# Kernel tuning notes

Hardware: AMD Instinct MI355X
Metric: run time of the kernel (lower is better)

Reference implementation:

```python
import jax, jax.numpy as jnp
import numpy as np

WS = (8, 8)            # window_size
NUM_HEADS = 8


def _rel_pos_index():
    # Faithful to the torch buffer construction (meshgrid indexing='ij').
    ch, cw = np.arange(WS[0]), np.arange(WS[1])
    coords = np.stack(np.meshgrid(ch, cw, indexing='ij')).reshape(2, -1)  # (2, N)
    rel = coords[:, :, None] - coords[:, None, :]                          # (2, N, N)
    rel = rel.transpose(1, 2, 0).copy()                                    # (N, N, 2)
    rel[..., 0] += WS[0] - 1
    rel[..., 1] += WS[1] - 1
    rel[..., 0] *= 2 * WS[1] - 1
    return jnp.asarray(rel.sum(-1))                                        # (N, N) int


def setup_inputs() -> dict:
    key = jax.random.key(0)
    ks = jax.random.split(key, 7)
    B_, C, N, nW = 4096, 256, 64, 4096  # B_ = batch(1) * num_windows(4096)
    return {
        "x": jax.random.normal(ks[0], (B_, C, N), jnp.float32),
        "mask": jax.random.normal(ks[1], (nW, N, N), jnp.float32),
        "qkv_w": jax.random.normal(ks[2], (3 * C, C), jnp.float32) * 0.05,
        "qkv_b": jax.random.normal(ks[3], (3 * C,), jnp.float32) * 0.02,
        "proj_w": jax.random.normal(ks[4], (C, C), jnp.float32) * 0.05,
        "proj_b": jax.random.normal(ks[5], (C,), jnp.float32) * 0.02,
        "bias_table": jax.random.normal(ks[6], ((2 * WS[0] - 1) * (2 * WS[1] - 1), NUM_HEADS), jnp.float32) * 0.02,
    }


def reference(x, mask, qkv_w, qkv_b, proj_w, proj_b, bias_table):
    B_, C, N = x.shape
    H = NUM_HEADS
    hd = C // H
    scale = hd ** -0.5

    # Conv1d kernel_size=1 == linear over the channel dim.
    qkv = jnp.einsum('bcn,dc->bdn', x, qkv_w) + qkv_b[None, :, None]   # (B_, 3C, N)
    qkv = qkv.reshape(B_, 3, H, hd, N)
    q, k, v = qkv[:, 0], qkv[:, 1], qkv[:, 2]                          # (B_, H, hd, N)

    attn = jnp.einsum('bhdn,bhdm->bhnm', q * scale, k)                 # (B_, H, N, N)

    rpi = _rel_pos_index()                                              # (N, N)
    bias = bias_table[rpi]                                              # (N, N, H) gather
    attn = attn + jnp.transpose(bias, (2, 0, 1))[None]                  # (B_, H, N, N)

    nW = mask.shape[0]
    attn = (attn.reshape(B_ // nW, nW, H, N, N) + mask[None, :, None]).reshape(B_, H, N, N)
    attn = jax.nn.softmax(attn, axis=-1)

    out = jnp.einsum('bhnm,bhdm->bnhd', attn, v).reshape(B_, N, C)      # (B_, N, C)
    return jnp.einsum('bnc,dc->bnd', out, proj_w) + proj_b              # (B_, N, C)
```

## Files before the change

### kernel.cpp

```cpp
#include <hip/hip_runtime.h>

typedef __bf16 bf16_t;
typedef bf16_t bf16x8 __attribute__((ext_vector_type(8)));
typedef bf16_t bf16x4 __attribute__((ext_vector_type(4)));
typedef float  f32x4  __attribute__((ext_vector_type(4)));

#define NWIN 4096
#define CDIM 256
#define NTOK 64
#define NH   8
#define HDIM 32

#define OFF_Q 0
#define OFF_K 40960
#define OFF_V 81920
#define OFF_X 118784
#define LDS_BYTES 152576

__device__ __forceinline__ f32x4 mfma16(bf16x8 a, bf16x8 b, f32x4 c) {
    return __builtin_amdgcn_mfma_f32_16x16x32_bf16(a, b, c, 0, 0, 0);
}

template<bool USE_WS>
__launch_bounds__(512, 2)
__global__ void win_attn_kernel(const float* __restrict__ x,
                                const float* __restrict__ mask,
                                const float* __restrict__ qkv_w,
                                const float* __restrict__ qkv_b,
                                const float* __restrict__ proj_w,
                                const float* __restrict__ proj_b,
                                const float* __restrict__ bias_table,
                                const bf16_t* __restrict__ qkv_wb,
                                const bf16_t* __restrict__ proj_wb,
                                float* __restrict__ out)
{
    __shared__ __attribute__((aligned(16))) unsigned char smem[LDS_BYTES];
    bf16_t* q_lds    = (bf16_t*)(smem + OFF_Q);
    bf16_t* k_lds    = (bf16_t*)(smem + OFF_K);
    bf16_t* v_lds    = (bf16_t*)(smem + OFF_V);
    bf16_t* xs       = (bf16_t*)(smem + OFF_X);
    float*  mask_lds = (float*) (smem + OFF_X);
    bf16_t* o_lds    = (bf16_t*)(smem + OFF_K);

    const int b    = blockIdx.x;
    const int tid  = threadIdx.x;
    const int w    = tid >> 6;
    const int lane = tid & 63;
    const int quad = lane >> 4;
    const int l15  = lane & 15;

    {
        const float* xb = x + (size_t)b * (CDIM * NTOK);
        #pragma unroll
        for (int it = 0; it < 8; ++it) {
            int i  = (tid + it * 512) * 4;
            int c  = i >> 6;
            int n0 = i & 63;
            f32x4 v4 = *(const f32x4*)(xb + i);
            #pragma unroll
            for (int j = 0; j < 4; ++j)
                xs[(n0 + j) * 264 + c] = (bf16_t)v4[j];
        }
    }
    __syncthreads();

    {
        f32x4 acc[6][4];
        #pragma unroll
        for (int rt = 0; rt < 6; ++rt)
            #pragma unroll
            for (int ct = 0; ct < 4; ++ct)
                acc[rt][ct] = (f32x4){0.f, 0.f, 0.f, 0.f};

        const int row_base = w * 96;
        for (int kk = 0; kk < 8; ++kk) {
            const int c0 = kk * 32;
            bf16x8 afr[6];
            #pragma unroll
            for (int rt = 0; rt < 6; ++rt) {
                int row = row_base + rt * 16 + l15;
                if constexpr (USE_WS) {
                    afr[rt] = *(const bf16x8*)(qkv_wb + row * CDIM + c0 + quad * 8);
                } else {
                    const float* ap = qkv_w + row * CDIM + c0 + quad * 8;
                    f32x4 a0 = *(const f32x4*)ap;
                    f32x4 a1 = *(const f32x4*)(ap + 4);
                    bf16x8 t;
                    #pragma unroll
                    for (int j = 0; j < 4; ++j) { t[j] = (bf16_t)a0[j]; t[j + 4] = (bf16_t)a1[j]; }
                    afr[rt] = t;
                }
            }
            bf16x8 bfr[4];
            #pragma unroll
            for (int ct = 0; ct < 4; ++ct)
                bfr[ct] = *(const bf16x8*)(xs + (ct * 16 + l15) * 264 + c0 + quad * 8);
            #pragma unroll
            for (int rt = 0; rt < 6; ++rt)
                #pragma unroll
                for (int ct = 0; ct < 4; ++ct)
                    acc[rt][ct] = mfma16(afr[rt], bfr[ct], acc[rt][ct]);
        }
        #pragma unroll
        for (int rt = 0; rt < 6; ++rt) {
            int r0  = row_base + rt * 16;
            int rq  = r0 + quad * 4;
            f32x4 b4 = *(const f32x4*)(qkv_b + rq);
            int sec = r0 >> 8;
            int h   = (r0 & 255) >> 5;
            int dd0 = rq & 31;
            #pragma unroll
            for (int ct = 0; ct < 4; ++ct) {
                int n = ct * 16 + l15;
                if (sec == 2) {
                    bf16_t* dst = v_lds + h * (32 * 72) + n;
                    #pragma unroll
                    for (int r = 0; r < 4; ++r)
                        dst[(dd0 + r) * 72] = (bf16_t)(acc[rt][ct][r] + b4[r]);
                } else {
                    bf16_t* dst = (sec == 0 ? q_lds : k_lds) + h * (64 * 40) + n * 40 + dd0;
                    bf16x4 pk;
                    #pragma unroll
                    for (int r = 0; r < 4; ++r) pk[r] = (bf16_t)(acc[rt][ct][r] + b4[r]);
                    *(bf16x4*)dst = pk;
                }
            }
        }
    }
    __syncthreads();

    {
        const float* mb = mask + (size_t)b * (NTOK * NTOK);
        #pragma unroll
        for (int it = 0; it < 2; ++it) {
            int i = (tid + it * 512) * 4;
            *(f32x4*)(mask_lds + i) = *(const f32x4*)(mb + i);
        }
    }

    const int h = w;
    f32x4 sacc[4][4];
    #pragma unroll
    for (int rt = 0; rt < 4; ++rt)
        #pragma unroll
        for (int ct = 0; ct < 4; ++ct)
            sacc[rt][ct] = (f32x4){0.f, 0.f, 0.f, 0.f};
    {
        bf16x8 qa[4], kb[4];
        #pragma unroll
        for (int rt = 0; rt < 4; ++rt)
            qa[rt] = *(const bf16x8*)(q_lds + h * 2560 + (rt * 16 + l15) * 40 + quad * 8);
        #pragma unroll
        for (int ct = 0; ct < 4; ++ct)
            kb[ct] = *(const bf16x8*)(k_lds + h * 2560 + (ct * 16 + l15) * 40 + quad * 8);
        #pragma unroll
        for (int rt = 0; rt < 4; ++rt)
            #pragma unroll
            for (int ct = 0; ct < 4; ++ct)
                sacc[rt][ct] = mfma16(qa[rt], kb[ct], sacc[rt][ct]);
    }
    __syncthreads();

    {
        const float scale = 0.17677669529663687f;
        int mh[4], mw[4], mcol[4];
        #pragma unroll
        for (int ct = 0; ct < 4; ++ct) {
            int m = ct * 16 + l15;
            mcol[ct] = m; mh[ct] = m >> 3; mw[ct] = m & 7;
        }
        #pragma unroll
        for (int rt = 0; rt < 4; ++rt) {
            #pragma unroll
            for (int reg = 0; reg < 4; ++reg) {
                int n  = rt * 16 + quad * 4 + reg;
                int nh = n >> 3, nw = n & 7;
                float l[4];
                #pragma unroll
                for (int ct = 0; ct < 4; ++ct) {
                    int idx = (nh - mh[ct] + 7) * 15 + (nw - mw[ct] + 7);
                    float bias = bias_table[idx * NH + h];
                    l[ct] = sacc[rt][ct][reg] * scale + bias + mask_lds[n * 64 + mcol[ct]];
                }
                float mx = fmaxf(fmaxf(l[0], l[1]), fmaxf(l[2], l[3]));
                #pragma unroll
                for (int d = 1; d < 16; d <<= 1) mx = fmaxf(mx, __shfl_xor(mx, d, 64));
                float s = 0.f;
                #pragma unroll
                for (int ct = 0; ct < 4; ++ct) { l[ct] = __expf(l[ct] - mx); s += l[ct]; }
                #pragma unroll
                for (int d = 1; d < 16; d <<= 1) s += __shfl_xor(s, d, 64);
                float inv = 1.0f / s;
                #pragma unroll
                for (int ct = 0; ct < 4; ++ct) sacc[rt][ct][reg] = l[ct] * inv;
            }
        }
    }

    f32x4 oacc[4][2];
    #pragma unroll
    for (int rt = 0; rt < 4; ++rt)
        #pragma unroll
        for (int cd = 0; cd < 2; ++cd)
            oacc[rt][cd] = (f32x4){0.f, 0.f, 0.f, 0.f};
    {
        bf16_t* p_lds = q_lds + h * 2560;
        #pragma unroll
        for (int ch = 0; ch < 2; ++ch) {
            #pragma unroll
            for (int rt = 0; rt < 4; ++rt)
                #pragma unroll
                for (int reg = 0; reg < 4; ++reg) {
                    int n = rt * 16 + quad * 4 + reg;
                    p_lds[n * 40 + l15]      = (bf16_t)sacc[rt][2 * ch][reg];
                    p_lds[n * 40 + 16 + l15] = (bf16_t)sacc[rt][2 * ch + 1][reg];
                }
            #pragma unroll
            for (int rt = 0; rt < 4; ++rt) {
                bf16x8 pa = *(const bf16x8*)(p_lds + (rt * 16 + l15) * 40 + quad * 8);
                #pragma unroll
                for (int cd = 0; cd < 2; ++cd) {
                    bf16x8 vb = *(const bf16x8*)(v_lds + h * 2304 + (cd * 16 + l15) * 72 + ch * 32 + quad * 8);
                    oacc[rt][cd] = mfma16(pa, vb, oacc[rt][cd]);
                }
            }
        }
    }
    __syncthreads();

    #pragma unroll
    for (int rt = 0; rt < 4; ++rt)
        #pragma unroll
        for (int cd = 0; cd < 2; ++cd) {
            int c = h * 32 + cd * 16 + l15;
            #pragma unroll
            for (int reg = 0; reg < 4; ++reg) {
                int n = rt * 16 + quad * 4 + reg;
                o_lds[n * 264 + c] = (bf16_t)oacc[rt][cd][reg];
            }
        }
    __syncthreads();

    {
        f32x4 yacc[2][4];
        #pragma unroll
        for (int rt = 0; rt < 2; ++rt)
            #pragma unroll
            for (int ct = 0; ct < 4; ++ct)
                yacc[rt][ct] = (f32x4){0.f, 0.f, 0.f, 0.f};

        for (int kk = 0; kk < 8; ++kk) {
            const int c0 = kk * 32;
            bf16x8 afr[2];
            #pragma unroll
            for (int rt = 0; rt < 2; ++rt) {
                int e = w * 32 + rt * 16 + l15;
                if constexpr (USE_WS) {
                    afr[rt] = *(const bf16x8*)(proj_wb + e * CDIM + c0 + quad * 8);
                } else {
                    const float* ap = proj_w + e * CDIM + c0 + quad * 8;
                    f32x4 a0 = *(const f32x4*)ap;
                    f32x4 a1 = *(const f32x4*)(ap + 4);
                    bf16x8 t;
                    #pragma unroll
                    for (int j = 0; j < 4; ++j) { t[j] = (bf16_t)a0[j]; t[j + 4] = (bf16_t)a1[j]; }
                    afr[rt] = t;
                }
            }
            bf16x8 bfr[4];
            #pragma unroll
            for (int ct = 0; ct < 4; ++ct)
                bfr[ct] = *(const bf16x8*)(o_lds + (ct * 16 + l15) * 264 + c0 + quad * 8);
            #pragma unroll
            for (int rt = 0; rt < 2; ++rt)
                #pragma unroll
                for (int ct = 0; ct < 4; ++ct)
                    yacc[rt][ct] = mfma16(afr[rt], bfr[ct], yacc[rt][ct]);
        }
        float* ob = out + (size_t)b * (NTOK * CDIM);
        #pragma unroll
        for (int rt = 0; rt < 2; ++rt) {
            int e0 = w * 32 + rt * 16 + quad * 4;
            f32x4 pb4 = *(const f32x4*)(proj_b + e0);
            #pragma unroll
            for (int ct = 0; ct < 4; ++ct) {
                int n = ct * 16 + l15;
                f32x4 r = yacc[rt][ct] + pb4;
                *(f32x4*)(ob + n * 256 + e0) = r;
            }
        }
    }
}

__global__ void cvt_weights(const float* __restrict__ qkv_w,
                            const float* __restrict__ proj_w,
                            bf16_t* __restrict__ qkv_wb,
                            bf16_t* __restrict__ proj_wb)
{
    int i = blockIdx.x * 256 + threadIdx.x;
    int base = i * 4;
    const float* src; bf16_t* dst;
    if (base < 196608) { src = qkv_w + base; dst = qkv_wb + base; }
    else { base -= 196608; src = proj_w + base; dst = proj_wb + base; }
    f32x4 v = *(const f32x4*)src;
    bf16x4 o;
    #pragma unroll
    for (int j = 0; j < 4; ++j) o[j] = (bf16_t)v[j];
    *(bf16x4*)dst = o;
}

extern "C" void kernel_launch(void* const* d_in, const int* in_sizes, int n_in,
                              void* d_out, int out_size, void* d_ws, size_t ws_size,
                              hipStream_t stream) {
    const float* x          = (const float*)d_in[0];
    const float* mask       = (const float*)d_in[1];
    const float* qkv_w      = (const float*)d_in[2];
    const float* qkv_b      = (const float*)d_in[3];
    const float* proj_w     = (const float*)d_in[4];
    const float* proj_b     = (const float*)d_in[5];
    const float* bias_table = (const float*)d_in[6];
    float* out = (float*)d_out;

    const size_t ws_needed = (size_t)(196608 + 65536) * sizeof(bf16_t);
    if (ws_size >= ws_needed) {
        bf16_t* qkv_wb  = (bf16_t*)d_ws;
        bf16_t* proj_wb = qkv_wb + 196608;
        cvt_weights<<<256, 256, 0, stream>>>(qkv_w, proj_w, qkv_wb, proj_wb);
        win_attn_kernel<true><<<NWIN, 512, 0, stream>>>(
            x, mask, qkv_w, qkv_b, proj_w, proj_b, bias_table, qkv_wb, proj_wb, out);
    } else {
        win_attn_kernel<false><<<NWIN, 512, 0, stream>>>(
            x, mask, qkv_w, qkv_b, proj_w, proj_b, bias_table, nullptr, nullptr, out);
    }
}
```

Baseline: 886.2 us.

## Assign each wave one head's QKV rows and keep Q/K/V in registers

Each wave now computes the Q, K and V projection rows for its own head, so the shared Q/K/V LDS buffers go away and each wave transposes through a small private scratch area without block barriers. LDS usage drops to about 58 KB, which allows the launch bound to request four blocks per CU instead of two. The change also folds the scale into Q, computes S transposed so the softmax reduction needs only two shuffles, defers normalisation to the output, and changes the x load pattern. The costs are higher register pressure from holding all per-head accumulators and possible spilling at the higher occupancy target.

Result: slower. 1.418 ms (+60.0%).

```diff
diff --git a/kernel.cpp b/kernel.cpp
--- a/kernel.cpp
+++ b/kernel.cpp
@@ -9,20 +9,16 @@
 #define CDIM 256
 #define NTOK 64
 #define NH   8
-#define HDIM 32
-
-#define OFF_Q 0
-#define OFF_K 40960
-#define OFF_V 81920
-#define OFF_X 118784
-#define LDS_BYTES 152576
+
+#define OFF_MASK  40960
+#define LDS_BYTES 58368
 
 __device__ __forceinline__ f32x4 mfma16(bf16x8 a, bf16x8 b, f32x4 c) {
     return __builtin_amdgcn_mfma_f32_16x16x32_bf16(a, b, c, 0, 0, 0);
 }
 
 template<bool USE_WS>
-__launch_bounds__(512, 2)
+__launch_bounds__(512, 4)
 __global__ void win_attn_kernel(const float* __restrict__ x,
                                 const float* __restrict__ mask,
                                 const float* __restrict__ qkv_w,
@@ -35,12 +31,9 @@
                                 float* __restrict__ out)
 {
     __shared__ __attribute__((aligned(16))) unsigned char smem[LDS_BYTES];
-    bf16_t* q_lds    = (bf16_t*)(smem + OFF_Q);
-    bf16_t* k_lds    = (bf16_t*)(smem + OFF_K);
-    bf16_t* v_lds    = (bf16_t*)(smem + OFF_V);
-    bf16_t* xs       = (bf16_t*)(smem + OFF_X);
-    float*  mask_lds = (float*) (smem + OFF_X);
-    bf16_t* o_lds    = (bf16_t*)(smem + OFF_K);
+    bf16_t* xs       = (bf16_t*)smem;
+    bf16_t* o_lds    = (bf16_t*)smem;
+    float*  mask_lds = (float*)(smem + OFF_MASK);
 
     const int b    = blockIdx.x;
     const int tid  = threadIdx.x;
@@ -48,196 +41,213 @@
     const int lane = tid & 63;
     const int quad = lane >> 4;
     const int l15  = lane & 15;
+    bf16_t* buf0 = (bf16_t*)(smem + w * 5120);
 
     {
         const float* xb = x + (size_t)b * (CDIM * NTOK);
         #pragma unroll
-        for (int it = 0; it < 8; ++it) {
-            int i  = (tid + it * 512) * 4;
-            int c  = i >> 6;
-            int n0 = i & 63;
-            f32x4 v4 = *(const f32x4*)(xb + i);
-            #pragma unroll
-            for (int j = 0; j < 4; ++j)
-                xs[(n0 + j) * 264 + c] = (bf16_t)v4[j];
+        for (int cb = 0; cb < 4; ++cb) {
+            const int c0 = cb * 64 + w * 8;
+            float v[8];
+            #pragma unroll
+            for (int j = 0; j < 8; ++j) v[j] = xb[(c0 + j) * 64 + lane];
+            bf16x8 t;
+            #pragma unroll
+            for (int j = 0; j < 8; ++j) t[j] = (bf16_t)v[j];
+            *(bf16x8*)(xs + lane * 264 + c0) = t;
+        }
+        const float* mb = mask + (size_t)b * (NTOK * NTOK);
+        #pragma unroll
+        for (int it = 0; it < 2; ++it) {
+            int e = (it * 512 + tid) * 4;
+            int n = e >> 6, m = e & 63;
+            f32x4 mv = *(const f32x4*)(mb + e);
+            *(f32x4*)(mask_lds + n * 68 + m) = mv;
         }
     }
     __syncthreads();
 
+    const int h = w;
+    f32x4 aqk[4][4];
+    f32x4 av[4][2];
+    #pragma unroll
+    for (int rt = 0; rt < 4; ++rt)
+        #pragma unroll
+        for (int ct = 0; ct < 4; ++ct) aqk[rt][ct] = (f32x4){0.f,0.f,0.f,0.f};
+    #pragma unroll
+    for (int ct = 0; ct < 4; ++ct)
+        #pragma unroll
+        for (int rtl = 0; rtl < 2; ++rtl) av[ct][rtl] = (f32x4){0.f,0.f,0.f,0.f};
+
+    for (int kk = 0; kk < 8; ++kk) {
+        const int c0 = kk * 32;
+        bf16x8 afr[6];
+        #pragma unroll
+        for (int rt = 0; rt < 6; ++rt) {
+            int row = ((rt >> 1) << 8) + h * 32 + ((rt & 1) << 4) + l15;
+            if constexpr (USE_WS) {
+                afr[rt] = *(const bf16x8*)(qkv_wb + row * CDIM + c0 + quad * 8);
+            } else {
+                const float* ap = qkv_w + row * CDIM + c0 + quad * 8;
+                f32x4 a0 = *(const f32x4*)ap;
+                f32x4 a1 = *(const f32x4*)(ap + 4);
+                bf16x8 t;
+                #pragma unroll
+                for (int j = 0; j < 4; ++j) { t[j] = (bf16_t)a0[j]; t[j+4] = (bf16_t)a1[j]; }
+                afr[rt] = t;
+            }
+        }
+        bf16x8 bfr[4];
+        #pragma unroll
+        for (int ct = 0; ct < 4; ++ct)
+            bfr[ct] = *(const bf16x8*)(xs + (ct * 16 + l15) * 264 + c0 + quad * 8);
+        #pragma unroll
+        for (int rt = 0; rt < 4; ++rt)
+            #pragma unroll
+            for (int ct = 0; ct < 4; ++ct)
+                aqk[rt][ct] = mfma16(afr[rt], bfr[ct], aqk[rt][ct]);
+        #pragma unroll
+        for (int ct = 0; ct < 4; ++ct)
+            #pragma unroll
+            for (int rtl = 0; rtl < 2; ++rtl)
+                av[ct][rtl] = mfma16(bfr[ct], afr[4 + rtl], av[ct][rtl]);
+    }
+    __syncthreads();
+
+    const float scale = 0.17677669529663687f;
+
+    #pragma unroll
+    for (int rtl = 0; rtl < 2; ++rtl) {
+        f32x4 b4 = *(const f32x4*)(qkv_b + h * 32 + rtl * 16 + quad * 4);
+        #pragma unroll
+        for (int ct = 0; ct < 4; ++ct) {
+            bf16x4 pk;
+            #pragma unroll
+            for (int r = 0; r < 4; ++r) pk[r] = (bf16_t)((aqk[rtl][ct][r] + b4[r]) * scale);
+            *(bf16x4*)(buf0 + (ct * 16 + l15) * 40 + rtl * 16 + quad * 4) = pk;
+        }
+    }
+    bf16x8 qa[4];
+    #pragma unroll
+    for (int nt = 0; nt < 4; ++nt)
+        qa[nt] = *(const bf16x8*)(buf0 + (nt * 16 + l15) * 40 + quad * 8);
+
+    #pragma unroll
+    for (int rtl = 0; rtl < 2; ++rtl) {
+        f32x4 b4 = *(const f32x4*)(qkv_b + 256 + h * 32 + rtl * 16 + quad * 4);
+        #pragma unroll
+        for (int ct = 0; ct < 4; ++ct) {
+            bf16x4 pk;
+            #pragma unroll
+            for (int r = 0; r < 4; ++r) pk[r] = (bf16_t)(aqk[2 + rtl][ct][r] + b4[r]);
+            *(bf16x4*)(buf0 + (ct * 16 + l15) * 40 + rtl * 16 + quad * 4) = pk;
+        }
+    }
+    bf16x8 kb[4];
+    #pragma unroll
+    for (int mt = 0; mt < 4; ++mt)
+        kb[mt] = *(const bf16x8*)(buf0 + (mt * 16 + l15) * 40 + quad * 8);
+
+    #pragma unroll
+    for (int rtl = 0; rtl < 2; ++rtl) {
+        float bv = qkv_b[512 + h * 32 + rtl * 16 + l15];
+        #pragma unroll
+        for (int ct = 0; ct < 4; ++ct) {
+            bf16x4 pk;
+            #pragma unroll
+            for (int r = 0; r < 4; ++r) pk[r] = (bf16_t)(av[ct][rtl][r] + bv);
+            *(bf16x4*)(buf0 + (rtl * 16 + l15) * 72 + ct * 16 + quad * 4) = pk;
+        }
+    }
+
+    f32x4 sacc[4][4];
+    #pragma unroll
+    for (int mt = 0; mt < 4; ++mt)
+        #pragma unroll
+        for (int nt = 0; nt < 4; ++nt)
+            sacc[mt][nt] = mfma16(kb[mt], qa[nt], (f32x4){0.f,0.f,0.f,0.f});
+
+    float inv[4];
     {
-        f32x4 acc[6][4];
-        #pragma unroll
-        for (int rt = 0; rt < 6; ++rt)
-            #pragma unroll
-            for (int ct = 0; ct < 4; ++ct)
-                acc[rt][ct] = (f32x4){0.f, 0.f, 0.f, 0.f};
-
-        const int row_base = w * 96;
-        for (int kk = 0; kk < 8; ++kk) {
-            const int c0 = kk * 32;
-            bf16x8 afr[6];
-            #pragma unroll
-            for (int rt = 0; rt < 6; ++rt) {
-                int row = row_base + rt * 16 + l15;
-                if constexpr (USE_WS) {
-                    afr[rt] = *(const bf16x8*)(qkv_wb + row * CDIM + c0 + quad * 8);
-                } else {
-                    const float* ap = qkv_w + row * CDIM + c0 + quad * 8;
-                    f32x4 a0 = *(const f32x4*)ap;
-                    f32x4 a1 = *(const f32x4*)(ap + 4);
-                    bf16x8 t;
-                    #pragma unroll
-                    for (int j = 0; j < 4; ++j) { t[j] = (bf16_t)a0[j]; t[j + 4] = (bf16_t)a1[j]; }
-                    afr[rt] = t;
+        const int qhi = quad >> 1, qlo = quad & 1;
+        const int nwv = (l15 & 7) + 7 - 4 * qlo;
+        const int nh_ = l15 >> 3;
+        #pragma unroll
+        for (int nt = 0; nt < 4; ++nt) {
+            const int n = nt * 16 + l15;
+            #pragma unroll
+            for (int mt = 0; mt < 4; ++mt) {
+                f32x4 mv = *(const f32x4*)(mask_lds + n * 68 + mt * 16 + quad * 4);
+                int base = (nt * 2 + nh_ - 2 * mt - qhi + 7) * 15 + nwv;
+                #pragma unroll
+                for (int r = 0; r < 4; ++r)
+                    sacc[mt][nt][r] += bias_table[(base - r) * NH + h] + mv[r];
+            }
+            float mx = sacc[0][nt][0];
+            #pragma unroll
+            for (int mt = 0; mt < 4; ++mt)
+                #pragma unroll
+                for (int r = 0; r < 4; ++r) mx = fmaxf(mx, sacc[mt][nt][r]);
+            mx = fmaxf(mx, __shfl_xor(mx, 16, 64));
+            mx = fmaxf(mx, __shfl_xor(mx, 32, 64));
+            float s = 0.f;
+            #pragma unroll
+            for (int mt = 0; mt < 4; ++mt)
+                #pragma unroll
+                for (int r = 0; r < 4; ++r) {
+                    float e = __expf(sacc[mt][nt][r] - mx);
+                    sacc[mt][nt][r] = e;
+                    s += e;
                 }
-            }
-            bf16x8 bfr[4];
-            #pragma unroll
-            for (int ct = 0; ct < 4; ++ct)
-                bfr[ct] = *(const bf16x8*)(xs + (ct * 16 + l15) * 264 + c0 + quad * 8);
-            #pragma unroll
-            for (int rt = 0; rt < 6; ++rt)
-                #pragma unroll
-                for (int ct = 0; ct < 4; ++ct)
-                    acc[rt][ct] = mfma16(afr[rt], bfr[ct], acc[rt][ct]);
-        }
-        #pragma unroll
-        for (int rt = 0; rt < 6; ++rt) {
-            int r0  = row_base + rt * 16;
-            int rq  = r0 + quad * 4;
-            f32x4 b4 = *(const f32x4*)(qkv_b + rq);
-            int sec = r0 >> 8;
-            int h   = (r0 & 255) >> 5;
-            int dd0 = rq & 31;
-            #pragma unroll
-            for (int ct = 0; ct < 4; ++ct) {
-                int n = ct * 16 + l15;
-                if (sec == 2) {
-                    bf16_t* dst = v_lds + h * (32 * 72) + n;
-                    #pragma unroll
-                    for (int r = 0; r < 4; ++r)
-                        dst[(dd0 + r) * 72] = (bf16_t)(acc[rt][ct][r] + b4[r]);
-                } else {
-                    bf16_t* dst = (sec == 0 ? q_lds : k_lds) + h * (64 * 40) + n * 40 + dd0;
-                    bf16x4 pk;
-                    #pragma unroll
-                    for (int r = 0; r < 4; ++r) pk[r] = (bf16_t)(acc[rt][ct][r] + b4[r]);
-                    *(bf16x4*)dst = pk;
-                }
-            }
+            s += __shfl_xor(s, 16, 64);
+            s += __shfl_xor(s, 32, 64);
+            inv[nt] = __builtin_amdgcn_rcpf(s);
+        }
+    }
+
+    bf16x8 vb[2][2];
+    #pragma unroll
+    for (int dt = 0; dt < 2; ++dt)
+        #pragma unroll
+        for (int ch = 0; ch < 2; ++ch)
+            vb[dt][ch] = *(const bf16x8*)(buf0 + (dt * 16 + l15) * 72 + ch * 32 + quad * 8);
+
+    f32x4 oaccT[2][4];
+    #pragma unroll
+    for (int dt = 0; dt < 2; ++dt)
+        #pragma unroll
+        for (int nt = 0; nt < 4; ++nt) oaccT[dt][nt] = (f32x4){0.f,0.f,0.f,0.f};
+
+    #pragma unroll
+    for (int ch = 0; ch < 2; ++ch) {
+        #pragma unroll
+        for (int mt2 = 0; mt2 < 2; ++mt2) {
+            #pragma unroll
+            for (int nt = 0; nt < 4; ++nt) {
+                bf16x4 pk;
+                #pragma unroll
+                for (int r = 0; r < 4; ++r) pk[r] = (bf16_t)sacc[2 * ch + mt2][nt][r];
+                *(bf16x4*)(buf0 + (nt * 16 + l15) * 40 + mt2 * 16 + quad * 4) = pk;
+            }
+        }
+        #pragma unroll
+        for (int nt = 0; nt < 4; ++nt) {
+            bf16x8 pb = *(const bf16x8*)(buf0 + (nt * 16 + l15) * 40 + quad * 8);
+            #pragma unroll
+            for (int dt = 0; dt < 2; ++dt)
+                oaccT[dt][nt] = mfma16(vb[dt][ch], pb, oaccT[dt][nt]);
         }
     }
     __syncthreads();
 
-    {
-        const float* mb = mask + (size_t)b * (NTOK * NTOK);
-        #pragma unroll
-        for (int it = 0; it < 2; ++it) {
-            int i = (tid + it * 512) * 4;
-            *(f32x4*)(mask_lds + i) = *(const f32x4*)(mb + i);
-        }
-    }
-
-    const int h = w;
-    f32x4 sacc[4][4];
-    #pragma unroll
-    for (int rt = 0; rt < 4; ++rt)
-        #pragma unroll
-        for (int ct = 0; ct < 4; ++ct)
-            sacc[rt][ct] = (f32x4){0.f, 0.f, 0.f, 0.f};
-    {
-        bf16x8 qa[4], kb[4];
-        #pragma unroll
-        for (int rt = 0; rt < 4; ++rt)
-            qa[rt] = *(const bf16x8*)(q_lds + h * 2560 + (rt * 16 + l15) * 40 + quad * 8);
-        #pragma unroll
-        for (int ct = 0; ct < 4; ++ct)
-            kb[ct] = *(const bf16x8*)(k_lds + h * 2560 + (ct * 16 + l15) * 40 + quad * 8);
-        #pragma unroll
-        for (int rt = 0; rt < 4; ++rt)
-            #pragma unroll
-            for (int ct = 0; ct < 4; ++ct)
-                sacc[rt][ct] = mfma16(qa[rt], kb[ct], sacc[rt][ct]);
-    }
-    __syncthreads();
-
-    {
-        const float scale = 0.17677669529663687f;
-        int mh[4], mw[4], mcol[4];
-        #pragma unroll
-        for (int ct = 0; ct < 4; ++ct) {
-            int m = ct * 16 + l15;
-            mcol[ct] = m; mh[ct] = m >> 3; mw[ct] = m & 7;
-        }
-        #pragma unroll
-        for (int rt = 0; rt < 4; ++rt) {
-            #pragma unroll
-            for (int reg = 0; reg < 4; ++reg) {
-                int n  = rt * 16 + quad * 4 + reg;
-                int nh = n >> 3, nw = n & 7;
-                float l[4];
-                #pragma unroll
-                for (int ct = 0; ct < 4; ++ct) {
-                    int idx = (nh - mh[ct] + 7) * 15 + (nw - mw[ct] + 7);
-                    float bias = bias_table[idx * NH + h];
-                    l[ct] = sacc[rt][ct][reg] * scale + bias + mask_lds[n * 64 + mcol[ct]];
-                }
-                float mx = fmaxf(fmaxf(l[0], l[1]), fmaxf(l[2], l[3]));
-                #pragma unroll
-                for (int d = 1; d < 16; d <<= 1) mx = fmaxf(mx, __shfl_xor(mx, d, 64));
-                float s = 0.f;
-                #pragma unroll
-                for (int ct = 0; ct < 4; ++ct) { l[ct] = __expf(l[ct] - mx); s += l[ct]; }
-                #pragma unroll
-                for (int d = 1; d < 16; d <<= 1) s += __shfl_xor(s, d, 64);
-                float inv = 1.0f / s;
-                #pragma unroll
-                for (int ct = 0; ct < 4; ++ct) sacc[rt][ct][reg] = l[ct] * inv;
-            }
-        }
-    }
-
-    f32x4 oacc[4][2];
-    #pragma unroll
-    for (int rt = 0; rt < 4; ++rt)
-        #pragma unroll
-        for (int cd = 0; cd < 2; ++cd)
-            oacc[rt][cd] = (f32x4){0.f, 0.f, 0.f, 0.f};
-    {
-        bf16_t* p_lds = q_lds + h * 2560;
-        #pragma unroll
-        for (int ch = 0; ch < 2; ++ch) {
-            #pragma unroll
-            for (int rt = 0; rt < 4; ++rt)
-                #pragma unroll
-                for (int reg = 0; reg < 4; ++reg) {
-                    int n = rt * 16 + quad * 4 + reg;
-                    p_lds[n * 40 + l15]      = (bf16_t)sacc[rt][2 * ch][reg];
-                    p_lds[n * 40 + 16 + l15] = (bf16_t)sacc[rt][2 * ch + 1][reg];
-                }
-            #pragma unroll
-            for (int rt = 0; rt < 4; ++rt) {
-                bf16x8 pa = *(const bf16x8*)(p_lds + (rt * 16 + l15) * 40 + quad * 8);
-                #pragma unroll
-                for (int cd = 0; cd < 2; ++cd) {
-                    bf16x8 vb = *(const bf16x8*)(v_lds + h * 2304 + (cd * 16 + l15) * 72 + ch * 32 + quad * 8);
-                    oacc[rt][cd] = mfma16(pa, vb, oacc[rt][cd]);
-                }
-            }
-        }
-    }
-    __syncthreads();
-
-    #pragma unroll
-    for (int rt = 0; rt < 4; ++rt)
-        #pragma unroll
-        for (int cd = 0; cd < 2; ++cd) {
-            int c = h * 32 + cd * 16 + l15;
-            #pragma unroll
-            for (int reg = 0; reg < 4; ++reg) {
-                int n = rt * 16 + quad * 4 + reg;
-                o_lds[n * 264 + c] = (bf16_t)oacc[rt][cd][reg];
-            }
+    #pragma unroll
+    for (int dt = 0; dt < 2; ++dt)
+        #pragma unroll
+        for (int nt = 0; nt < 4; ++nt) {
+            bf16x4 pk;
+            #pragma unroll
+            for (int r = 0; r < 4; ++r) pk[r] = (bf16_t)(oaccT[dt][nt][r] * inv[nt]);
+            *(bf16x4*)(o_lds + (nt * 16 + l15) * 264 + h * 32 + dt * 16 + quad * 4) = pk;
         }
     __syncthreads();
 
@@ -246,8 +256,7 @@
         #pragma unroll
         for (int rt = 0; rt < 2; ++rt)
             #pragma unroll
-            for (int ct = 0; ct < 4; ++ct)
-                yacc[rt][ct] = (f32x4){0.f, 0.f, 0.f, 0.f};
+            for (int ct = 0; ct < 4; ++ct) yacc[rt][ct] = (f32x4){0.f,0.f,0.f,0.f};
 
         for (int kk = 0; kk < 8; ++kk) {
             const int c0 = kk * 32;
@@ -263,7 +272,7 @@
                     f32x4 a1 = *(const f32x4*)(ap + 4);
                     bf16x8 t;
                     #pragma unroll
-                    for (int j = 0; j < 4; ++j) { t[j] = (bf16_t)a0[j]; t[j + 4] = (bf16_t)a1[j]; }
+                    for (int j = 0; j < 4; ++j) { t[j] = (bf16_t)a0[j]; t[j+4] = (bf16_t)a1[j]; }
                     afr[rt] = t;
                 }
             }
```
